# Optimization experiments

Measured on AMD Instinct MI355X. Metric: run time of the kernel, lower is better.

The kernel has to match this reference:

```python
import jax, jax.numpy as jnp
import numpy as np

N, M, Z_DIM = 32768, 8192, 256

def setup_inputs() -> dict:
    key = jax.random.key(0)
    k1, k2 = jax.random.split(key)
    mean = jax.random.normal(k1, (N, Z_DIM), dtype=jnp.float32)
    e = jax.random.normal(k2, (M, Z_DIM), dtype=jnp.float32)
    return {"mean": mean, "e": e, "sigma": 1}

def reference(mean, e, sigma):
    sigma = jnp.float32(sigma)
    # squared pairwise distance via ||a||^2 + ||b||^2 - 2 a.b (avoids (N,M,Z) broadcast)
    a2 = jnp.sum(mean * mean, axis=1, keepdims=True)          # (N, 1)
    b2 = jnp.sum(e * e, axis=1)[None, :]                      # (1, M)
    ab = jnp.einsum('nd,md->nm', mean, e)                     # (N, M)
    distance = a2 + b2 - 2.0 * ab                             # (N, M)
    logits = (-1.0 / (2.0 * sigma * sigma)) * distance
    # logsumexp over the N axis (dim=0), mean over the M samples
    loss = -jnp.mean(jax.nn.logsumexp(logits, axis=0))
    return loss
```

## Files before the change

kernel.cpp:

```cpp
#include <hip/hip_runtime.h>
#include <hip/hip_bf16.h>
#include <cstdint>
#include <cstddef>

#define Z 256
#define CG 128
#define RT 64
#define NCH 8
#define LOG2E 1.4426950408889634f
#define LN2 0.6931471805599453f

typedef __attribute__((ext_vector_type(4))) float f32x4;
typedef long long fp8v8;

#define GLOAD_LDS16(g, l)                                                              \
  __builtin_amdgcn_global_load_lds((const __attribute__((address_space(1))) void*)(g), \
                                   (__attribute__((address_space(3))) void*)(l), 16, 0, 0)

__device__ __forceinline__ float fast_exp2(float x) {
#if __has_builtin(__builtin_amdgcn_exp2f)
  return __builtin_amdgcn_exp2f(x);
#else
  float r;
  asm("v_exp_f32 %0, %1" : "=v"(r) : "v"(x));
  return r;
#endif
}

__global__ __launch_bounds__(256) void prep_kernel(const float* __restrict__ mean,
                                                   const float* __restrict__ e,
                                                   unsigned char* __restrict__ Abf,
                                                   unsigned char* __restrict__ Bbf,
                                                   float* __restrict__ nrm,
                                                   const int* __restrict__ sigma_p,
                                                   int Nr, int Mr) {
  const float sgm = (float)(*sigma_p);
  const float c1 = LOG2E / (sgm * sgm);
  const float k2 = 0.5f * c1;
  const float sc = sqrtf(c1);
  const int tid = threadIdx.x;
  const int lane32 = tid & 31;
  const int row = blockIdx.x * 8 + (tid >> 5);
  if (row >= Nr + Mr) return;
  const float* src = (row < Nr) ? (mean + (size_t)row * Z) : (e + (size_t)(row - Nr) * Z);
  unsigned char* d = (row < Nr) ? (Abf + (size_t)row * Z) : (Bbf + (size_t)(row - Nr) * Z);
  const float4 v0 = *reinterpret_cast<const float4*>(src + lane32 * 8);
  const float4 v1 = *reinterpret_cast<const float4*>(src + lane32 * 8 + 4);
  float s = v0.x * v0.x + v0.y * v0.y + v0.z * v0.z + v0.w * v0.w +
            v1.x * v1.x + v1.y * v1.y + v1.z * v1.z + v1.w * v1.w;
  s += __shfl_xor(s, 1); s += __shfl_xor(s, 2); s += __shfl_xor(s, 4);
  s += __shfl_xor(s, 8); s += __shfl_xor(s, 16);
  if (lane32 == 0) nrm[row] = k2 * s;
  int r0 = __builtin_amdgcn_cvt_pk_fp8_f32(v0.x * sc, v0.y * sc, 0, false);
  r0 = __builtin_amdgcn_cvt_pk_fp8_f32(v0.z * sc, v0.w * sc, r0, true);
  int r1 = __builtin_amdgcn_cvt_pk_fp8_f32(v1.x * sc, v1.y * sc, 0, false);
  r1 = __builtin_amdgcn_cvt_pk_fp8_f32(v1.z * sc, v1.w * sc, r1, true);
  *reinterpret_cast<int2*>(d + lane32 * 8) = make_int2(r0, r1);
}

#define STAGE_TILE(BUF, T)                                  \
  {                                                         \
    const char* g = Ab8 + (size_t)(T) * 16384;              \
    GLOAD_LDS16(g + gof0, Sb + (BUF) * 16384 + o0);         \
    GLOAD_LDS16(g + gof1, Sb + (BUF) * 16384 + o1);         \
  }

#define COMPUTE_TILE(BUF)                                                               \
  {                                                                                     \
    _Pragma("unroll") for (int kk = 0; kk < 8; ++kk) {                                  \
      fp8v8 afr[2];                                                                     \
      const int s8 = kk * 4 + laneHi;                                                   \
      _Pragma("unroll") for (int a = 0; a < 2; ++a) {                                   \
        const int ro = wr * 32 + a * 16 + laneLo;                                       \
        const int addr = ro * 256 + ((((s8 >> 1) ^ (ro & 7)) << 4) | ((s8 & 1) << 3));  \
        afr[a] = *reinterpret_cast<const fp8v8*>(Sb + (BUF) * 16384 + addr);            \
      }                                                                                 \
      _Pragma("unroll") for (int a = 0; a < 2; ++a)                                     \
          _Pragma("unroll") for (int c = 0; c < 2; ++c)                                 \
              acc[a][c] = __builtin_amdgcn_mfma_f32_16x16x32_fp8_fp8(                   \
                  afr[a], bfr[c][kk],                                                   \
                  (kk == 0) ? f32x4{0.f, 0.f, 0.f, 0.f} : acc[a][c], 0, 0, 0);          \
    }                                                                                   \
  }

#define EPILOGUE                                                                      \
  {                                                                                   \
    _Pragma("unroll") for (int c = 0; c < 2; ++c) {                                   \
      float w0 = acc[0][c][0] - av0.x, w1 = acc[0][c][1] - av0.y;                     \
      float w2 = acc[0][c][2] - av0.z, w3 = acc[0][c][3] - av0.w;                     \
      float w4 = acc[1][c][0] - av1.x, w5 = acc[1][c][1] - av1.y;                     \
      float w6 = acc[1][c][2] - av1.z, w7 = acc[1][c][3] - av1.w;                     \
      float mx = fmaxf(fmaxf(fmaxf(w0, w1), fmaxf(w2, w3)),                           \
                       fmaxf(fmaxf(w4, w5), fmaxf(w6, w7)));                          \
      float nm = fmaxf(m_run[c], mx);                                                 \
      float ss = fast_exp2(w0 - nm) + fast_exp2(w1 - nm) + fast_exp2(w2 - nm) +       \
                 fast_exp2(w3 - nm) + fast_exp2(w4 - nm) + fast_exp2(w5 - nm) +       \
                 fast_exp2(w6 - nm) + fast_exp2(w7 - nm);                             \
      s_run[c] = s_run[c] * fast_exp2(m_run[c] - nm) + ss;                            \
      m_run[c] = nm;                                                                  \
    }                                                                                 \
  }

#define ALOAD                                                  \
  av0 = *reinterpret_cast<const float4*>(aptr);                \
  av1 = *reinterpret_cast<const float4*>(aptr + 16);           \
  aptr += 64;

__global__ __launch_bounds__(512, 4) void gemm_lse_kernel(
    const unsigned char* __restrict__ Abf,
    const unsigned char* __restrict__ Bbf,
    const float* __restrict__ nrm,
    float2* __restrict__ part,
    int Mtot, int chRows) {
  __shared__ __align__(16) char Sb[32768];

  const int tid = threadIdx.x;
  const int lane = tid & 63;
  const int w = tid >> 6;
  const int wr = w >> 2, wc = w & 3;
  const int laneLo = lane & 15, laneHi = lane >> 4;

  const int id = blockIdx.x;
  const int y = id & 7;
  const int x = id >> 3;
  const int row0base = y * chRows;
  const int col0 = x * CG;
  const int ntiles = chRows / RT;

#pragma unroll
  for (int i = 0; i < 4; ++i) {
    int o = i * 8192 + tid * 16;
    int r = o >> 8;
    int p = (o >> 4) & 15;
    GLOAD_LDS16((const char*)Bbf + (size_t)(col0 + r) * Z + ((p ^ (r & 7)) << 4),
                Sb + o);
  }
  __syncthreads();
  fp8v8 bfr[2][8];
#pragma unroll
  for (int c = 0; c < 2; ++c) {
    const int rb = wc * 32 + c * 16 + laneLo;
#pragma unroll
    for (int kk = 0; kk < 8; ++kk) {
      const int s8 = kk * 4 + laneHi;
      const int addr = rb * 256 + ((((s8 >> 1) ^ (rb & 7)) << 4) | ((s8 & 1) << 3));
      bfr[c][kk] = *reinterpret_cast<const fp8v8*>(Sb + addr);
    }
  }
  __syncthreads();

  const char* Ab8 = (const char*)Abf + (size_t)row0base * Z;
  const int o0 = tid * 16, o1 = 8192 + tid * 16;
  const int r_0 = o0 >> 8, p_0 = (o0 >> 4) & 15;
  const int r_1 = o1 >> 8, p_1 = (o1 >> 4) & 15;
  const int gof0 = r_0 * 256 + ((p_0 ^ (r_0 & 7)) << 4);
  const int gof1 = r_1 * 256 + ((p_1 ^ (r_1 & 7)) << 4);
  const float* aptr = nrm + row0base + wr * 32 + laneHi * 4;

  f32x4 acc[2][2];
  float m_run[2] = {-1e30f, -1e30f};
  float s_run[2] = {0.f, 0.f};
  float4 av0, av1;

  STAGE_TILE(0, 0);
  __syncthreads();

  for (int tp = 0; tp < ntiles / 2; ++tp) {
    const int t = tp * 2;
    STAGE_TILE(1, t + 1);
    ALOAD;
    COMPUTE_TILE(0);
    EPILOGUE;
    __syncthreads();
    if (tp + 1 < ntiles / 2) STAGE_TILE(0, t + 2);
    ALOAD;
    COMPUTE_TILE(1);
    EPILOGUE;
    __syncthreads();
  }

  float* redM = (float*)Sb;
  float* redS = (float*)(Sb + 1024);
#pragma unroll
  for (int c = 0; c < 2; ++c) {
#pragma unroll
    for (int off = 16; off <= 32; off <<= 1) {
      float om = __shfl_xor(m_run[c], off);
      float os = __shfl_xor(s_run[c], off);
      float nm = fmaxf(m_run[c], om);
      s_run[c] = s_run[c] * fast_exp2(m_run[c] - nm) + os * fast_exp2(om - nm);
      m_run[c] = nm;
    }
    if (laneHi == 0) {
      redM[wr * 128 + wc * 32 + c * 16 + laneLo] = m_run[c];
      redS[wr * 128 + wc * 32 + c * 16 + laneLo] = s_run[c];
    }
  }
  __syncthreads();
  if (tid < CG) {
    float m0 = redM[tid], m1 = redM[128 + tid];
    float s0 = redS[tid], s1 = redS[128 + tid];
    float Mx = fmaxf(m0, m1);
    float Sx = s0 * fast_exp2(m0 - Mx) + s1 * fast_exp2(m1 - Mx);
    part[(size_t)y * Mtot + col0 + tid] = make_float2(Mx, Sx);
  }
}

__global__ __launch_bounds__(256) void lse_finish(const float2* __restrict__ part,
                                                  const float* __restrict__ bLp,
                                                  int NB, int Mtot,
                                                  float* __restrict__ out) {
  const int m = blockIdx.x * blockDim.x + threadIdx.x;
  float mx = -1e30f, s = 0.f;
  for (int b = 0; b < NB; ++b) {
    float2 p = part[(size_t)b * Mtot + m];
    float nm = fmaxf(mx, p.x);
    s = s * fast_exp2(mx - nm) + p.y * fast_exp2(p.x - nm);
    mx = nm;
  }
  float v = mx + __log2f(s) - bLp[m];
#pragma unroll
  for (int off = 32; off >= 1; off >>= 1) v += __shfl_xor(v, off);
  __shared__ float red[4];
  if ((threadIdx.x & 63) == 0) red[threadIdx.x >> 6] = v;
  __syncthreads();
  if (threadIdx.x == 0)
    atomicAdd(out, -LN2 * (red[0] + red[1] + red[2] + red[3]) / (float)Mtot);
}

extern "C" void kernel_launch(void* const* d_in, const int* in_sizes, int n_in,
                              void* d_out, int out_size, void* d_ws, size_t ws_size,
                              hipStream_t stream) {
  const float* mean = (const float*)d_in[0];
  const float* e    = (const float*)d_in[1];
  const int* sigma  = (const int*)d_in[2];
  const int N_ = in_sizes[0] / Z;
  const int M_ = in_sizes[1] / Z;
  const int chRows = N_ / NCH;

  char* ws = (char*)d_ws;
  unsigned char* Abf = (unsigned char*)ws; ws += (size_t)N_ * Z;
  unsigned char* Bbf = (unsigned char*)ws; ws += (size_t)M_ * Z;
  float* nrm = (float*)ws;                 ws += (size_t)(N_ + M_) * sizeof(float);
  float2* part = (float2*)ws;

  hipMemsetAsync(d_out, 0, sizeof(float), stream);
  prep_kernel<<<(N_ + M_) / 8, 256, 0, stream>>>(mean, e, Abf, Bbf, nrm, sigma, N_, M_);
  gemm_lse_kernel<<<(M_ / CG) * NCH, 512, 0, stream>>>(Abf, Bbf, nrm, part, M_, chRows);
  lse_finish<<<M_ / 256, 256, 0, stream>>>(part, nrm + N_, NCH, M_, (float*)d_out);
}
```

Measured before the change: 185.4 us.

## Permute fp8 K layout for 16-byte LDS reads, double row chunks and occupancy

The prep kernel now writes fp8 rows in a permuted K order so each lane's two consecutive MFMA K-slices are contiguous. The GEMM then loads them with one 16-byte LDS read instead of two 8-byte reads, for both the A tiles and the B fragments. The row dimension is split into 16 chunks instead of 8 to create more blocks, and the launch bounds request 8 blocks per CU. The costs are more partial logsumexp results to combine, and a tighter register budget that could cause spills.

```diff
diff --git a/kernel.cpp b/kernel.cpp
--- a/kernel.cpp
+++ b/kernel.cpp
@@ -6,12 +6,13 @@
 #define Z 256
 #define CG 128
 #define RT 64
-#define NCH 8
+#define NCH 16
 #define LOG2E 1.4426950408889634f
 #define LN2 0.6931471805599453f
 
 typedef __attribute__((ext_vector_type(4))) float f32x4;
 typedef long long fp8v8;
+typedef __attribute__((ext_vector_type(2))) long long fp8v16;
 
 #define GLOAD_LDS16(g, l)                                                              \
   __builtin_amdgcn_global_load_lds((const __attribute__((address_space(1))) void*)(g), \
@@ -55,7 +56,8 @@
   r0 = __builtin_amdgcn_cvt_pk_fp8_f32(v0.z * sc, v0.w * sc, r0, true);
   int r1 = __builtin_amdgcn_cvt_pk_fp8_f32(v1.x * sc, v1.y * sc, 0, false);
   r1 = __builtin_amdgcn_cvt_pk_fp8_f32(v1.z * sc, v1.w * sc, r1, true);
-  *reinterpret_cast<int2*>(d + lane32 * 8) = make_int2(r0, r1);
+  *reinterpret_cast<int2*>(d + ((lane32 & 3) << 6) + ((lane32 >> 2) << 3)) =
+      make_int2(r0, r1);
 }
 
 #define STAGE_TILE(BUF, T)                                  \
@@ -65,22 +67,25 @@
     GLOAD_LDS16(g + gof1, Sb + (BUF) * 16384 + o1);         \
   }
 
-#define COMPUTE_TILE(BUF)                                                               \
-  {                                                                                     \
-    _Pragma("unroll") for (int kk = 0; kk < 8; ++kk) {                                  \
-      fp8v8 afr[2];                                                                     \
-      const int s8 = kk * 4 + laneHi;                                                   \
-      _Pragma("unroll") for (int a = 0; a < 2; ++a) {                                   \
-        const int ro = wr * 32 + a * 16 + laneLo;                                       \
-        const int addr = ro * 256 + ((((s8 >> 1) ^ (ro & 7)) << 4) | ((s8 & 1) << 3));  \
-        afr[a] = *reinterpret_cast<const fp8v8*>(Sb + (BUF) * 16384 + addr);            \
-      }                                                                                 \
-      _Pragma("unroll") for (int a = 0; a < 2; ++a)                                     \
-          _Pragma("unroll") for (int c = 0; c < 2; ++c)                                 \
-              acc[a][c] = __builtin_amdgcn_mfma_f32_16x16x32_fp8_fp8(                   \
-                  afr[a], bfr[c][kk],                                                   \
-                  (kk == 0) ? f32x4{0.f, 0.f, 0.f, 0.f} : acc[a][c], 0, 0, 0);          \
-    }                                                                                   \
+#define COMPUTE_TILE(BUF)                                                             \
+  {                                                                                   \
+    _Pragma("unroll") for (int kp = 0; kp < 4; ++kp) {                                \
+      fp8v16 at[2];                                                                   \
+      const int slot = laneHi * 4 + kp;                                               \
+      _Pragma("unroll") for (int a = 0; a < 2; ++a) {                                 \
+        const int ro = wr * 32 + a * 16 + laneLo;                                     \
+        at[a] = *reinterpret_cast<const fp8v16*>(                                     \
+            Sb + (BUF) * 16384 + ro * 256 + ((slot ^ (ro & 7)) << 4));                \
+      }                                                                               \
+      _Pragma("unroll") for (int a = 0; a < 2; ++a)                                   \
+          _Pragma("unroll") for (int c = 0; c < 2; ++c) {                             \
+        acc[a][c] = __builtin_amdgcn_mfma_f32_16x16x32_fp8_fp8(                       \
+            at[a][0], bfr[c][2 * kp],                                                 \
+            (kp == 0) ? f32x4{0.f, 0.f, 0.f, 0.f} : acc[a][c], 0, 0, 0);              \
+        acc[a][c] = __builtin_amdgcn_mfma_f32_16x16x32_fp8_fp8(                       \
+            at[a][1], bfr[c][2 * kp + 1], acc[a][c], 0, 0, 0);                        \
+      }                                                                               \
+    }                                                                                 \
   }
 
 #define EPILOGUE                                                                      \
@@ -106,7 +111,7 @@
   av1 = *reinterpret_cast<const float4*>(aptr + 16);           \
   aptr += 64;
 
-__global__ __launch_bounds__(512, 4) void gemm_lse_kernel(
+__global__ __launch_bounds__(512, 8) void gemm_lse_kernel(
     const unsigned char* __restrict__ Abf,
     const unsigned char* __restrict__ Bbf,
     const float* __restrict__ nrm,
@@ -121,8 +126,8 @@
   const int laneLo = lane & 15, laneHi = lane >> 4;
 
   const int id = blockIdx.x;
-  const int y = id & 7;
-  const int x = id >> 3;
+  const int y = id & 15;
+  const int x = id >> 4;
   const int row0base = y * chRows;
   const int col0 = x * CG;
   const int ntiles = chRows / RT;
@@ -141,10 +146,12 @@
   for (int c = 0; c < 2; ++c) {
     const int rb = wc * 32 + c * 16 + laneLo;
 #pragma unroll
-    for (int kk = 0; kk < 8; ++kk) {
-      const int s8 = kk * 4 + laneHi;
-      const int addr = rb * 256 + ((((s8 >> 1) ^ (rb & 7)) << 4) | ((s8 & 1) << 3));
-      bfr[c][kk] = *reinterpret_cast<const fp8v8*>(Sb + addr);
+    for (int kp = 0; kp < 4; ++kp) {
+      const int slot = laneHi * 4 + kp;
+      fp8v16 v = *reinterpret_cast<const fp8v16*>(Sb + rb * 256 +
+                                                  ((slot ^ (rb & 7)) << 4));
+      bfr[c][2 * kp] = v[0];
+      bfr[c][2 * kp + 1] = v[1];
     }
   }
   __syncthreads();
```

Result: slower. 412.8 us (+122.6%).
